# Optimization experiments

Measured on AMD Instinct MI355X. Metric: run time of the kernel, lower is better.

## Reference

```python
import jax, jax.numpy as jnp
import numpy as np

D = 128
N = 262144

def setup_inputs() -> dict:
    key = jax.random.key(0)
    ks = jax.random.split(key, 10)
    inp = {
        'member_embeddings': 0.1 * jax.random.normal(ks[0], (N, D), dtype=jnp.float32),
        'item_embedding': 0.1 * jax.random.normal(ks[1], (D,), dtype=jnp.float32),
        # nn.Linear params (torch convention: y = x @ W.T + b)
        'W_c1': jax.random.normal(ks[2], (D, D), dtype=jnp.float32) / np.sqrt(D),
        'b_c1': jnp.zeros((D,), dtype=jnp.float32),
        'W_c2': jax.random.normal(ks[3], (D, D), dtype=jnp.float32) / np.sqrt(D),
        'b_c2': jnp.zeros((D,), dtype=jnp.float32),
        'w_pa': jax.random.normal(ks[4], (D,), dtype=jnp.float32) / np.sqrt(D),  # peer_attention weight (1,D) squeezed
        'b_pa': jnp.zeros((), dtype=jnp.float32),
        'w_vc': jax.random.normal(ks[5], (D,), dtype=jnp.float32) / np.sqrt(D),  # v_c weight (1,D) squeezed
        'b_vc': jnp.zeros((), dtype=jnp.float32),
    }
    return inp

def reference(member_embeddings, item_embedding, W_c1, b_c1, W_c2, b_c2, w_pa, b_pa, w_vc, b_vc):
    E = member_embeddings  # [N, D]
    # SP: self persistence scores  alpha_SP_i = u_i^T v
    sp = E @ item_embedding  # [N]
    # Peer scores are per-member scalars shared across all exclusion sets.
    s = E @ w_pa + b_pa                       # [N]
    m = jnp.max(s)
    e = jnp.exp(s - m)                        # [N]
    S = jnp.sum(e)                            # scalar
    eE = e[:, None] * E                       # [N, D]
    sum_eE = jnp.sum(eE, axis=0)              # [D]
    # softmax over peers excluding i (exact: softmax is shift-invariant)
    denom = S - e                             # [N]
    peer_agg = (sum_eE[None, :] - eE) / denom[:, None]  # [N, D]
    # PI: v_c^T ReLU(W_c1 u_i + W_c2 peer_agg_i + b)
    h = E @ W_c1.T + b_c1 + peer_agg @ W_c2.T + b_c2     # [N, D]
    pi = jax.nn.relu(h) @ w_vc + b_vc                    # [N]  (dropout = identity in eval)
    alpha = jnp.float32(1.0)
    beta = jnp.float32(1.0)
    attention_weights = jax.nn.softmax(alpha * sp + beta * pi, axis=0)  # [N]
    group_embedding = attention_weights @ E               # [D]
    return (group_embedding, attention_weights)
```

## Files before the change

### kernel.cpp

```cpp
#include <hip/hip_runtime.h>
#include <hip/hip_bf16.h>

#define DIM 128

typedef __attribute__((ext_vector_type(8))) short bf16x8;
typedef __attribute__((ext_vector_type(4))) float f32x4;

#define WS_B12    0
#define WS_C      128
#define WS_SUMEE  256
#define WS_S      384
#define WS_ZB     416
#define WS_GEB    512
#define WS_WBF    4608
#define WS_EEP    20992
#define WS_SEP    152064
#define WS_SP     153088
#define WS_E      415232
#define WS_WEXP   677376
#define WS_EBF    939520

__device__ __forceinline__ unsigned short f2bf(float f) {
    union { float f; unsigned u; } v; v.f = f;
    unsigned r = v.u + 0x7fffu + ((v.u >> 16) & 1u);
    return (unsigned short)(r >> 16);
}

__device__ __forceinline__ float bfbits(unsigned u) {
    union { unsigned u; float f; } v; v.u = u;
    return v.f;
}

__device__ __forceinline__ unsigned pkbf(float a, float b) {
    union { __hip_bfloat162 h; unsigned u; } cv;
    cv.h = __float22bfloat162_rn(make_float2(a, b));
    return cv.u;
}

__global__ __launch_bounds__(256) void k2_stats(const float* __restrict__ E,
                                                const float* __restrict__ v,
                                                const float* __restrict__ wpa,
                                                const float* __restrict__ bpa,
                                                const float* __restrict__ Wc1,
                                                const float* __restrict__ Wc2,
                                                const float* __restrict__ bc1,
                                                const float* __restrict__ bc2,
                                                float* __restrict__ ws) {
    __shared__ float red[16][128];
    __shared__ float redS[16];
    int t = threadIdx.x;

    int gid = blockIdx.x * 256 + t;
    unsigned short* wbf_w = (unsigned short*)(ws + WS_WBF);
    if (gid < 32768) {
        int n = gid >> 7, k = gid & 127;
        float val = (n < 128) ? Wc1[n * 128 + k] : Wc2[(n - 128) * 128 + k];
        wbf_w[gid] = f2bf(val);
    }
    if (gid < 4096) ws[WS_GEB + gid] = 0.f;
    if (gid < 128) ws[WS_B12 + gid] = bc1[gid] + bc2[gid];
    if (gid < 64) ws[WS_ZB + gid] = 0.f;

    int wave = t >> 6, lane = t & 63;
    int cl = lane & 15, rs = lane >> 4;
    int row0 = blockIdx.x * 256;
    const float4* E4 = (const float4*)E;
    unsigned short* ebf = (unsigned short*)(ws + WS_EBF);

    float4 va = ((const float4*)v)[cl];
    float4 vb = ((const float4*)v)[16 + cl];
    float4 pa = ((const float4*)wpa)[cl];
    float4 pb = ((const float4*)wpa)[16 + cl];
    float bias = bpa[0];

    float4 acc0 = {0.f, 0.f, 0.f, 0.f}, acc1 = {0.f, 0.f, 0.f, 0.f};
    float se = 0.f;
    float* sp_ws = ws + WS_SP;
    float* e_ws = ws + WS_E;

#pragma unroll 8
    for (int it = 0; it < 16; ++it) {
        int row = row0 + it * 16 + wave * 4 + rs;
        float4 x0 = E4[row * 32 + cl];
        float4 x1 = E4[row * 32 + 16 + cl];
        unsigned p0 = pkbf(x0.x, x0.y);
        unsigned p1 = pkbf(x0.z, x0.w);
        unsigned p2 = pkbf(x1.x, x1.y);
        unsigned p3 = pkbf(x1.z, x1.w);
        *(uint2*)(ebf + (size_t)row * 128 + cl * 4) = make_uint2(p0, p1);
        *(uint2*)(ebf + (size_t)row * 128 + 64 + cl * 4) = make_uint2(p2, p3);

        float dv = x0.x * va.x + x0.y * va.y + x0.z * va.z + x0.w * va.w
                 + x1.x * vb.x + x1.y * vb.y + x1.z * vb.z + x1.w * vb.w;
        float dp = x0.x * pa.x + x0.y * pa.y + x0.z * pa.z + x0.w * pa.w
                 + x1.x * pb.x + x1.y * pb.y + x1.z * pb.z + x1.w * pb.w;
        for (int off = 1; off < 16; off <<= 1) {
            dv += __shfl_xor(dv, off);
            dp += __shfl_xor(dp, off);
        }
        float e = __expf(dp + bias);
        if (cl == 0) {
            sp_ws[row] = dv;
            e_ws[row] = e;
            se += e;
        }
        acc0.x += e * x0.x; acc0.y += e * x0.y; acc0.z += e * x0.z; acc0.w += e * x0.w;
        acc1.x += e * x1.x; acc1.y += e * x1.y; acc1.z += e * x1.z; acc1.w += e * x1.w;
    }
    int rr = wave * 4 + rs;
    float* dst = red[rr];
    dst[cl * 4 + 0] = acc0.x; dst[cl * 4 + 1] = acc0.y;
    dst[cl * 4 + 2] = acc0.z; dst[cl * 4 + 3] = acc0.w;
    dst[64 + cl * 4 + 0] = acc1.x; dst[64 + cl * 4 + 1] = acc1.y;
    dst[64 + cl * 4 + 2] = acc1.z; dst[64 + cl * 4 + 3] = acc1.w;
    if (cl == 0) redS[rr] = se;
    __syncthreads();
    if (t < 128) {
        float s = 0.f;
#pragma unroll
        for (int r = 0; r < 16; ++r) s += red[r][t];
        ws[WS_EEP + t * 1024 + blockIdx.x] = s;
    }
    if (t == 0) {
        float s = 0.f;
#pragma unroll
        for (int r = 0; r < 16; ++r) s += redS[r];
        ws[WS_SEP + blockIdx.x] = s;
    }
}

__global__ __launch_bounds__(256) void k2b_reduce(float* __restrict__ ws) {
    __shared__ float r4[4];
    int t = threadIdx.x, blk = blockIdx.x;
    const float* src = (blk < 128) ? (ws + WS_EEP + blk * 1024) : (ws + WS_SEP);
    float s = src[t] + src[t + 256] + src[t + 512] + src[t + 768];
    for (int off = 1; off < 64; off <<= 1) s += __shfl_xor(s, off);
    if ((t & 63) == 0) r4[t >> 6] = s;
    __syncthreads();
    if (t == 0) {
        float tot = r4[0] + r4[1] + r4[2] + r4[3];
        if (blk < 128) ws[WS_SUMEE + blk] = tot;
        else ws[WS_S] = tot;
    }
}

__global__ __launch_bounds__(256, 2) void k4_main(const float* __restrict__ wvc,
                                                  const float* __restrict__ bvc_p,
                                                  const float* __restrict__ Wc2,
                                                  float* __restrict__ ws) {
    __shared__ unsigned short Elds[3][64 * 136];
    __shared__ __align__(16) float arena[644];
    float* pim2  = arena;
    float* c_lds = arena + 512;
    float* zw    = arena + 640;
    float* gep_a = arena;

    int t = threadIdx.x;
    int w = t >> 6, lane = t & 63, cl = lane & 15, q = lane >> 4;
    int blk = blockIdx.x;
    int row_base = blk * 512;
    const unsigned short* wbf = (const unsigned short*)(ws + WS_WBF);
    const unsigned short* EbBase = (const unsigned short*)(ws + WS_EBF);
    const float* e_ws = ws + WS_E;

    float bvc = bvc_p[0];
    float Sv = ws[WS_S];
    int r0 = w * 16 + q * 4;
    int sr0 = t >> 4,           sc0 = t & 15;
    int sr1 = (t + 256) >> 4,   sc1 = (t + 256) & 15;
    int sr2 = (t + 512) >> 4,   sc2 = (t + 512) & 15;
    int sr3 = (t + 768) >> 4,   sc3 = (t + 768) & 15;

    bf16x8 aw[2][2][4];
#pragma unroll
    for (int jt = 0; jt < 2; ++jt) {
#pragma unroll
        for (int kt = 0; kt < 4; ++kt) {
            int jrow = w * 32 + jt * 16 + cl;
            aw[jt][0][kt] = *(const bf16x8*)(wbf + jrow * 128 + kt * 32 + q * 8);
            aw[jt][1][kt] = *(const bf16x8*)(wbf + (128 + jrow) * 128 + kt * 32 + q * 8);
        }
    }

    float b12r[2][4], wvr[2][4];
#pragma unroll
    for (int jt = 0; jt < 2; ++jt)
#pragma unroll
        for (int reg = 0; reg < 4; ++reg) {
            int jr = w * 32 + jt * 16 + q * 4 + reg;
            b12r[jt][reg] = ws[WS_B12 + jr];
            wvr[jt][reg] = wvc[jr];
        }

    if (t < 128) {
        const float4* row = (const float4*)(Wc2 + t * 128);
        const float4* se4 = (const float4*)(ws + WS_SUMEE);
        float4 s4 = {0.f, 0.f, 0.f, 0.f};
#pragma unroll
        for (int k = 0; k < 32; ++k) {
            float4 a = row[k], b = se4[k];
            s4.x += a.x * b.x; s4.y += a.y * b.y; s4.z += a.z * b.z; s4.w += a.w * b.w;
        }
        c_lds[t] = s4.x + s4.y + s4.z + s4.w;
    }

    {
        const unsigned short* Eb0 = EbBase + (size_t)row_base * 128;
        uint4 a0 = *(const uint4*)(Eb0 + t * 8);
        uint4 a1 = *(const uint4*)(Eb0 + (t + 256) * 8);
        uint4 a2 = *(const uint4*)(Eb0 + (t + 512) * 8);
        uint4 a3 = *(const uint4*)(Eb0 + (t + 768) * 8);
        *(uint4*)&Elds[0][sr0 * 136 + sc0 * 8] = a0;
        *(uint4*)&Elds[0][sr1 * 136 + sc1 * 8] = a1;
        *(uint4*)&Elds[0][sr2 * 136 + sc2 * 8] = a2;
        *(uint4*)&Elds[0][sr3 * 136 + sc3 * 8] = a3;
    }
    uint4 sN0, sN1, sN2, sN3;
    {
        const unsigned short* Eb1 = EbBase + (size_t)(row_base + 64) * 128;
        sN0 = *(const uint4*)(Eb1 + t * 8);
        sN1 = *(const uint4*)(Eb1 + (t + 256) * 8);
        sN2 = *(const uint4*)(Eb1 + (t + 512) * 8);
        sN3 = *(const uint4*)(Eb1 + (t + 768) * 8);
    }
    __syncthreads();

    float cjr[2][4];
#pragma unroll
    for (int jt = 0; jt < 2; ++jt)
#pragma unroll
        for (int reg = 0; reg < 4; ++reg)
            cjr[jt][reg] = c_lds[w * 32 + jt * 16 + q * 4 + reg];

    float z_lane = 0.f;
    float acc8[8] = {0.f, 0.f, 0.f, 0.f, 0.f, 0.f, 0.f, 0.f};

    for (int it = 0; it < 8; ++it) {
        int cur = it % 3;
        int pb = it & 1;
        int trow0 = row_base + it * 64;

        if (it < 7) {
            int wr = (it + 1) % 3;
            *(uint4*)&Elds[wr][sr0 * 136 + sc0 * 8] = sN0;
            *(uint4*)&Elds[wr][sr1 * 136 + sc1 * 8] = sN1;
            *(uint4*)&Elds[wr][sr2 * 136 + sc2 * 8] = sN2;
            *(uint4*)&Elds[wr][sr3 * 136 + sc3 * 8] = sN3;
        }
        if (it < 6) {
            const unsigned short* EbN = EbBase + (size_t)(trow0 + 128) * 128;
            sN0 = *(const uint4*)(EbN + t * 8);
            sN1 = *(const uint4*)(EbN + (t + 256) * 8);
            sN2 = *(const uint4*)(EbN + (t + 512) * 8);
            sN3 = *(const uint4*)(EbN + (t + 768) * 8);
        }
        float4 sp4 = *(const float4*)&ws[WS_SP + trow0 + r0];
        float evr[4];
#pragma unroll
        for (int rt = 0; rt < 4; ++rt) evr[rt] = e_ws[trow0 + rt * 16 + cl];

        f32x4 acc[4][2][2];
#pragma unroll
        for (int rt = 0; rt < 4; ++rt)
#pragma unroll
            for (int jt = 0; jt < 2; ++jt) {
                acc[rt][jt][0] = (f32x4){0.f, 0.f, 0.f, 0.f};
                acc[rt][jt][1] = (f32x4){0.f, 0.f, 0.f, 0.f};
            }
#pragma unroll
        for (int rt = 0; rt < 4; ++rt) {
            bf16x8 b[4];
#pragma unroll
            for (int kt = 0; kt < 4; ++kt)
                b[kt] = *(const bf16x8*)&Elds[cur][(rt * 16 + cl) * 136 + kt * 32 + q * 8];
#pragma unroll
            for (int kt = 0; kt < 4; ++kt) {
                acc[rt][0][0] = __builtin_amdgcn_mfma_f32_16x16x32_bf16(aw[0][0][kt], b[kt], acc[rt][0][0], 0, 0, 0);
                acc[rt][0][1] = __builtin_amdgcn_mfma_f32_16x16x32_bf16(aw[0][1][kt], b[kt], acc[rt][0][1], 0, 0, 0);
                acc[rt][1][0] = __builtin_amdgcn_mfma_f32_16x16x32_bf16(aw[1][0][kt], b[kt], acc[rt][1][0], 0, 0, 0);
                acc[rt][1][1] = __builtin_amdgcn_mfma_f32_16x16x32_bf16(aw[1][1][kt], b[kt], acc[rt][1][1], 0, 0, 0);
            }
        }

#pragma unroll
        for (int rt = 0; rt < 4; ++rt) {
            float e_v = evr[rt];
            float di_v = 1.0f / (Sv - e_v);
            float p = 0.f;
#pragma unroll
            for (int jt = 0; jt < 2; ++jt)
#pragma unroll
                for (int reg = 0; reg < 4; ++reg) {
                    float h = acc[rt][jt][0][reg] + b12r[jt][reg]
                            + (cjr[jt][reg] - e_v * acc[rt][jt][1][reg]) * di_v;
                    p = fmaf(wvr[jt][reg], fmaxf(h, 0.f), p);
                }
            p += __shfl_xor(p, 16);
            p += __shfl_xor(p, 32);
            if (lane < 16) pim2[(pb * 64 + rt * 16 + lane) * 4 + w] = p;
        }
        __syncthreads();

        float we[4];
#pragma unroll
        for (int rr = 0; rr < 4; ++rr) {
            float4 P = *(const float4*)&pim2[(pb * 64 + r0 + rr) * 4];
            float pi = (P.x + P.y) + (P.z + P.w);
            float spv = (rr == 0) ? sp4.x : (rr == 1) ? sp4.y : (rr == 2) ? sp4.z : sp4.w;
            we[rr] = __expf(spv + bvc + pi);
            z_lane += we[rr];
        }
        if (cl == 0)
            *(float4*)&ws[WS_WEXP + trow0 + r0] = (float4){we[0], we[1], we[2], we[3]};

#pragma unroll
        for (int rr = 0; rr < 4; ++rr) {
            int r = r0 + rr;
            float wer = we[rr];
            uint4 u = *(const uint4*)&Elds[cur][r * 136 + cl * 8];
            acc8[0] += wer * bfbits(u.x << 16);
            acc8[1] += wer * bfbits(u.x & 0xffff0000u);
            acc8[2] += wer * bfbits(u.y << 16);
            acc8[3] += wer * bfbits(u.y & 0xffff0000u);
            acc8[4] += wer * bfbits(u.z << 16);
            acc8[5] += wer * bfbits(u.z & 0xffff0000u);
            acc8[6] += wer * bfbits(u.w << 16);
            acc8[7] += wer * bfbits(u.w & 0xffff0000u);
        }
    }

    __syncthreads();

    z_lane += __shfl_xor(z_lane, 16);
    z_lane += __shfl_xor(z_lane, 32);
    if (lane == 0) zw[w] = z_lane;

#pragma unroll
    for (int jj = 0; jj < 8; ++jj) {
        acc8[jj] += __shfl_xor(acc8[jj], 16);
        acc8[jj] += __shfl_xor(acc8[jj], 32);
    }
    if (lane < 16) {
        *(float4*)&gep_a[w * 128 + cl * 8] = (float4){acc8[0], acc8[1], acc8[2], acc8[3]};
        *(float4*)&gep_a[w * 128 + cl * 8 + 4] = (float4){acc8[4], acc8[5], acc8[6], acc8[7]};
    }
    __syncthreads();

    if (t < 128) {
        float tot = gep_a[t] + gep_a[128 + t] + gep_a[256 + t] + gep_a[384 + t];
        atomicAdd(&ws[WS_GEB + (blk & 31) * 128 + t], tot);
    }
    if (t == 128) {
        float zs = zw[0] + zw[1] + zw[2] + zw[3];
        atomicAdd(&ws[WS_ZB + (blk & 63)], zs);
    }
}

__global__ __launch_bounds__(256) void k5_final(const float* __restrict__ ws,
                                                float* __restrict__ out) {
    int t = threadIdx.x, blk = blockIdx.x;
    float z = ws[WS_ZB + (t & 63)];
    for (int off = 1; off < 64; off <<= 1) z += __shfl_xor(z, off);
    float invZ = 1.0f / z;
    if (blk < 1024) {
        int i = blk * 256 + t;
        out[128 + i] = ws[WS_WEXP + i] * invZ;
    } else if (t < 128) {
        float s = 0.f;
#pragma unroll
        for (int b = 0; b < 32; ++b) s += ws[WS_GEB + b * 128 + t];
        out[t] = s * invZ;
    }
}

extern "C" void kernel_launch(void* const* d_in, const int* in_sizes, int n_in,
                              void* d_out, int out_size, void* d_ws, size_t ws_size,
                              hipStream_t stream) {
    const float* E   = (const float*)d_in[0];
    const float* v   = (const float*)d_in[1];
    const float* Wc1 = (const float*)d_in[2];
    const float* bc1 = (const float*)d_in[3];
    const float* Wc2 = (const float*)d_in[4];
    const float* bc2 = (const float*)d_in[5];
    const float* wpa = (const float*)d_in[6];
    const float* bpa = (const float*)d_in[7];
    const float* wvc = (const float*)d_in[8];
    const float* bvc = (const float*)d_in[9];
    float* ws  = (float*)d_ws;
    float* out = (float*)d_out;

    k2_stats<<<1024, 256, 0, stream>>>(E, v, wpa, bpa, Wc1, Wc2, bc1, bc2, ws);
    k2b_reduce<<<129, 256, 0, stream>>>(ws);
    k4_main<<<512, 256, 0, stream>>>(wvc, bvc, Wc2, ws);
    k5_final<<<1025, 256, 0, stream>>>(ws, out);
}
```

Before: 253.5 us.

## Stream padded bf16 E tiles to LDS via global_load_lds and raise occupancy

k2_stats now writes the bf16 copy of E with a padded row stride of 136, matching the LDS tile layout. k4_main can then copy each 64-row tile straight from global memory into LDS with the gfx950 global_load_lds builtin, replacing the register-staged load/store pipeline. The per-rt MFMA accumulators are now consumed right away instead of being held for all four rt slices, which cuts register pressure. Launch bounds move to 3 blocks per SM and the grid doubles to 1024 blocks of 256 rows each. Trade-offs: the bf16 workspace grows, more per-block partials go to the final reduction, and the DMA path relies on the buffer rotation being properly synchronised.

```diff
diff --git a/kernel.cpp b/kernel.cpp
--- a/kernel.cpp
+++ b/kernel.cpp
@@ -87,8 +87,8 @@
         unsigned p1 = pkbf(x0.z, x0.w);
         unsigned p2 = pkbf(x1.x, x1.y);
         unsigned p3 = pkbf(x1.z, x1.w);
-        *(uint2*)(ebf + (size_t)row * 128 + cl * 4) = make_uint2(p0, p1);
-        *(uint2*)(ebf + (size_t)row * 128 + 64 + cl * 4) = make_uint2(p2, p3);
+        *(uint2*)(ebf + (size_t)row * 136 + cl * 4) = make_uint2(p0, p1);
+        *(uint2*)(ebf + (size_t)row * 136 + 64 + cl * 4) = make_uint2(p2, p3);
 
         float dv = x0.x * va.x + x0.y * va.y + x0.z * va.z + x0.w * va.w
                  + x1.x * vb.x + x1.y * vb.y + x1.z * vb.z + x1.w * vb.w;
@@ -144,7 +144,7 @@
     }
 }
 
-__global__ __launch_bounds__(256, 2) void k4_main(const float* __restrict__ wvc,
+__global__ __launch_bounds__(256, 3) void k4_main(const float* __restrict__ wvc,
                                                   const float* __restrict__ bvc_p,
                                                   const float* __restrict__ Wc2,
                                                   float* __restrict__ ws) {
@@ -158,18 +158,31 @@
     int t = threadIdx.x;
     int w = t >> 6, lane = t & 63, cl = lane & 15, q = lane >> 4;
     int blk = blockIdx.x;
-    int row_base = blk * 512;
+    int row_base = blk * 256;
     const unsigned short* wbf = (const unsigned short*)(ws + WS_WBF);
-    const unsigned short* EbBase = (const unsigned short*)(ws + WS_EBF);
+    const unsigned short* EbP = (const unsigned short*)(ws + WS_EBF);
     const float* e_ws = ws + WS_E;
 
     float bvc = bvc_p[0];
     float Sv = ws[WS_S];
     int r0 = w * 16 + q * 4;
-    int sr0 = t >> 4,           sc0 = t & 15;
-    int sr1 = (t + 256) >> 4,   sc1 = (t + 256) & 15;
-    int sr2 = (t + 512) >> 4,   sc2 = (t + 512) & 15;
-    int sr3 = (t + 768) >> 4,   sc3 = (t + 768) & 15;
+
+#define STAGE(buf, trow) do {                                                          \
+    const unsigned short* gs_ = EbP + (size_t)(trow) * 136;                            \
+    _Pragma("unroll")                                                                  \
+    for (int k_ = 0; k_ < 4; ++k_) {                                                   \
+        int c_ = w + k_ * 4;                                                           \
+        __builtin_amdgcn_global_load_lds(                                              \
+            (const __attribute__((address_space(1))) void*)(gs_ + c_ * 512 + lane * 8),\
+            (__attribute__((address_space(3))) void*)(&Elds[buf][c_ * 512]),           \
+            16, 0, 0);                                                                 \
+    }                                                                                  \
+    if (w == 0)                                                                        \
+        __builtin_amdgcn_global_load_lds(                                              \
+            (const __attribute__((address_space(1))) void*)(gs_ + 16 * 512 + lane * 8),\
+            (__attribute__((address_space(3))) void*)(&Elds[buf][16 * 512]),           \
+            16, 0, 0);                                                                 \
+} while (0)
 
     bf16x8 aw[2][2][4];
 #pragma unroll
@@ -204,25 +217,7 @@
         c_lds[t] = s4.x + s4.y + s4.z + s4.w;
     }
 
-    {
-        const unsigned short* Eb0 = EbBase + (size_t)row_base * 128;
-        uint4 a0 = *(const uint4*)(Eb0 + t * 8);
-        uint4 a1 = *(const uint4*)(Eb0 + (t + 256) * 8);
-        uint4 a2 = *(const uint4*)(Eb0 + (t + 512) * 8);
-        uint4 a3 = *(const uint4*)(Eb0 + (t + 768) * 8);
-        *(uint4*)&Elds[0][sr0 * 136 + sc0 * 8] = a0;
-        *(uint4*)&Elds[0][sr1 * 136 + sc1 * 8] = a1;
-        *(uint4*)&Elds[0][sr2 * 136 + sc2 * 8] = a2;
-        *(uint4*)&Elds[0][sr3 * 136 + sc3 * 8] = a3;
-    }
-    uint4 sN0, sN1, sN2, sN3;
-    {
-        const unsigned short* Eb1 = EbBase + (size_t)(row_base + 64) * 128;
-        sN0 = *(const uint4*)(Eb1 + t * 8);
-        sN1 = *(const uint4*)(Eb1 + (t + 256) * 8);
-        sN2 = *(const uint4*)(Eb1 + (t + 512) * 8);
-        sN3 = *(const uint4*)(Eb1 + (t + 768) * 8);
-    }
+    STAGE(0, row_base);
     __syncthreads();
 
     float cjr[2][4];
@@ -235,66 +230,46 @@
     float z_lane = 0.f;
     float acc8[8] = {0.f, 0.f, 0.f, 0.f, 0.f, 0.f, 0.f, 0.f};
 
-    for (int it = 0; it < 8; ++it) {
+    for (int it = 0; it < 4; ++it) {
         int cur = it % 3;
         int pb = it & 1;
         int trow0 = row_base + it * 64;
 
-        if (it < 7) {
-            int wr = (it + 1) % 3;
-            *(uint4*)&Elds[wr][sr0 * 136 + sc0 * 8] = sN0;
-            *(uint4*)&Elds[wr][sr1 * 136 + sc1 * 8] = sN1;
-            *(uint4*)&Elds[wr][sr2 * 136 + sc2 * 8] = sN2;
-            *(uint4*)&Elds[wr][sr3 * 136 + sc3 * 8] = sN3;
-        }
-        if (it < 6) {
-            const unsigned short* EbN = EbBase + (size_t)(trow0 + 128) * 128;
-            sN0 = *(const uint4*)(EbN + t * 8);
-            sN1 = *(const uint4*)(EbN + (t + 256) * 8);
-            sN2 = *(const uint4*)(EbN + (t + 512) * 8);
-            sN3 = *(const uint4*)(EbN + (t + 768) * 8);
-        }
+        if (it < 3) STAGE((it + 1) % 3, trow0 + 64);
+
         float4 sp4 = *(const float4*)&ws[WS_SP + trow0 + r0];
         float evr[4];
 #pragma unroll
         for (int rt = 0; rt < 4; ++rt) evr[rt] = e_ws[trow0 + rt * 16 + cl];
 
-        f32x4 acc[4][2][2];
-#pragma unroll
-        for (int rt = 0; rt < 4; ++rt)
-#pragma unroll
-            for (int jt = 0; jt < 2; ++jt) {
-                acc[rt][jt][0] = (f32x4){0.f, 0.f, 0.f, 0.f};
-                acc[rt][jt][1] = (f32x4){0.f, 0.f, 0.f, 0.f};
-            }
 #pragma unroll
         for (int rt = 0; rt < 4; ++rt) {
             bf16x8 b[4];
 #pragma unroll
             for (int kt = 0; kt < 4; ++kt)
                 b[kt] = *(const bf16x8*)&Elds[cur][(rt * 16 + cl) * 136 + kt * 32 + q * 8];
+            f32x4 a00 = {0.f,0.f,0.f,0.f}, a01 = {0.f,0.f,0.f,0.f};
+            f32x4 a10 = {0.f,0.f,0.f,0.f}, a11 = {0.f,0.f,0.f,0.f};
 #pragma unroll
             for (int kt = 0; kt < 4; ++kt) {
-                acc[rt][0][0] = __builtin_amdgcn_mfma_f32_16x16x32_bf16(aw[0][0][kt], b[kt], acc[rt][0][0], 0, 0, 0);
-                acc[rt][0][1] = __builtin_amdgcn_mfma_f32_16x16x32_bf16(aw[0][1][kt], b[kt], acc[rt][0][1], 0, 0, 0);
-                acc[rt][1][0] = __builtin_amdgcn_mfma_f32_16x16x32_bf16(aw[1][0][kt], b[kt], acc[rt][1][0], 0, 0, 0);
-                acc[rt][1][1] = __builtin_amdgcn_mfma_f32_16x16x32_bf16(aw[1][1][kt], b[kt], acc[rt][1][1], 0, 0, 0);
+                a00 = __builtin_amdgcn_mfma_f32_16x16x32_bf16(aw[0][0][kt], b[kt], a00, 0, 0, 0);
+                a01 = __builtin_amdgcn_mfma_f32_16x16x32_bf16(aw[0][1][kt], b[kt], a01, 0, 0, 0);
+                a10 = __builtin_amdgcn_mfma_f32_16x16x32_bf16(aw[1][0][kt], b[kt], a10, 0, 0, 0);
+                a11 = __builtin_amdgcn_mfma_f32_16x16x32_bf16(aw[1][1][kt], b[kt], a11, 0, 0, 0);
             }
-        }
-
-#pragma unroll
-        for (int rt = 0; rt < 4; ++rt) {
             float e_v = evr[rt];
             float di_v = 1.0f / (Sv - e_v);
             float p = 0.f;
 #pragma unroll
-            for (int jt = 0; jt < 2; ++jt)
-#pragma unroll
-                for (int reg = 0; reg < 4; ++reg) {
-                    float h = acc[rt][jt][0][reg] + b12r[jt][reg]
-                            + (cjr[jt][reg] - e_v * acc[rt][jt][1][reg]) * di_v;
-                    p = fmaf(wvr[jt][reg], fmaxf(h, 0.f), p);
-                }
+            for (int reg = 0; reg < 4; ++reg) {
+                float h = a00[reg] + b12r[0][reg] + (cjr[0][reg] - e_v * a01[reg]) * di_v;
+                p = fmaf(wvr[0][reg], fmaxf(h, 0.f), p);
+            }
+#pragma unroll
+            for (int reg = 0; reg < 4; ++reg) {
+                float h = a10[reg] + b12r[1][reg] + (cjr[1][reg] - e_v * a11[reg]) * di_v;
+                p = fmaf(wvr[1][reg], fmaxf(h, 0.f), p);
+            }
             p += __shfl_xor(p, 16);
             p += __shfl_xor(p, 32);
             if (lane < 16) pim2[(pb * 64 + rt * 16 + lane) * 4 + w] = p;
@@ -328,6 +303,7 @@
             acc8[7] += wer * bfbits(u.w & 0xffff0000u);
         }
     }
+#undef STAGE
 
     __syncthreads();
 
@@ -391,6 +367,6 @@
 
     k2_stats<<<1024, 256, 0, stream>>>(E, v, wpa, bpa, Wc1, Wc2, bc1, bc2, ws);
     k2b_reduce<<<129, 256, 0, stream>>>(ws);
-    k4_main<<<512, 256, 0, stream>>>(wvc, bvc, Wc2, ws);
+    k4_main<<<1024, 256, 0, stream>>>(wvc, bvc, Wc2, ws);
     k5_final<<<1025, 256, 0, stream>>>(ws, out);
 }
```

After: 269.2 us. 6.2% more time.
